# Kernel tuning notes

Measured on AMD Instinct MI355X. Metric: run time of the kernel, lower is better.

## Reference

```python
import jax, jax.numpy as jnp
import numpy as np

EPS = 1e-6


def layernorm(x, w, b):
    m = jnp.mean(x, axis=-1, keepdims=True)
    v = jnp.var(x, axis=-1, keepdims=True)
    return (x - m) * jax.lax.rsqrt(v + EPS) * w + b


def rotate_half(x):
    x1, x2 = jnp.split(x, 2, axis=-1)
    return jnp.concatenate((-x2, x1), axis=-1)


def setup_inputs() -> dict:
    key = jax.random.key(0)
    ks = jax.random.split(key, 16)
    T, D, H, HD, I = 16384, 1280, 16, 80, 5120
    NSEG = 16
    inp = {
        "hidden_states": jax.random.normal(ks[0], (T, D), jnp.float32),
        "cos": jax.random.uniform(ks[1], (T, HD), jnp.float32),
        "sin": jax.random.uniform(ks[2], (T, HD), jnp.float32),
        "ln1_w": jnp.ones((D,), jnp.float32),
        "ln1_b": jnp.zeros((D,), jnp.float32),
        "ln2_w": jnp.ones((D,), jnp.float32),
        "ln2_b": jnp.zeros((D,), jnp.float32),
        "qkv_w": jax.random.normal(ks[3], (3 * D, D), jnp.float32) * 0.02,
        "qkv_b": jnp.zeros((3 * D,), jnp.float32),
        "proj_w": jax.random.normal(ks[4], (D, D), jnp.float32) * 0.02,
        "proj_b": jnp.zeros((D,), jnp.float32),
        "fc1_w": jax.random.normal(ks[5], (I, D), jnp.float32) * 0.02,
        "fc1_b": jnp.zeros((I,), jnp.float32),
        "fc2_w": jax.random.normal(ks[6], (D, I), jnp.float32) * 0.02,
        "fc2_b": jnp.zeros((D,), jnp.float32),
        "cu_seqlens": jnp.arange(NSEG + 1, dtype=jnp.int32) * (T // NSEG),
    }
    return inp


def reference(hidden_states, cos, sin, ln1_w, ln1_b, ln2_w, ln2_b,
              qkv_w, qkv_b, proj_w, proj_b, fc1_w, fc1_b, fc2_w, fc2_b,
              cu_seqlens):
    T, D = hidden_states.shape
    H = 16
    HD = D // H
    nseg = cu_seqlens.shape[0] - 1  # equal-length segments by construction
    L = T // nseg

    x = layernorm(hidden_states, ln1_w, ln1_b)
    qkv = (x @ qkv_w.T + qkv_b).reshape(T, 3, H, HD)
    q, k, v = qkv[:, 0], qkv[:, 1], qkv[:, 2]  # [T, H, HD]

    # RoPE in fp32, cos/sin broadcast over heads
    c = cos[:, None, :]
    s = sin[:, None, :]
    q = q * c + rotate_half(q) * s
    k = k * c + rotate_half(k) * s

    # block-diagonal varlen attention: reshape into [nseg, L, H, HD]
    qs = q.reshape(nseg, L, H, HD)
    ks = k.reshape(nseg, L, H, HD)
    vs = v.reshape(nseg, L, H, HD)
    scale = 1.0 / jnp.sqrt(jnp.asarray(HD, jnp.float32))
    scores = jnp.einsum('slhd,smhd->shlm', qs, ks) * scale
    probs = jax.nn.softmax(scores, axis=-1)
    attn = jnp.einsum('shlm,smhd->slhd', probs, vs).reshape(T, D)

    attn_out = attn @ proj_w.T + proj_b
    h = hidden_states + attn_out

    y = layernorm(h, ln2_w, ln2_b)
    mlp = (jax.nn.silu(y @ fc1_w.T + fc1_b)) @ fc2_w.T + fc2_b
    return h + mlp
```

## Files before the change

kernel.cpp:

```cpp
#include <hip/hip_runtime.h>
#include <hip/hip_bf16.h>
#include <hip/hip_fp16.h>

typedef _Float16 f16;
typedef _Float16 f16x2 __attribute__((ext_vector_type(2)));
typedef _Float16 f16x4 __attribute__((ext_vector_type(4)));
typedef _Float16 f16x8 __attribute__((ext_vector_type(8)));
typedef float f32x4 __attribute__((ext_vector_type(4)));
typedef float f32x16 __attribute__((ext_vector_type(16)));
typedef int i32x4 __attribute__((ext_vector_type(4)));

#define T_TOK 16384
#define D_MOD 1280
#define N_QKV 3840
#define I_MLP 5120
#define N_HEAD 16
#define HD 80
#define SEG_L 1024

__device__ __forceinline__ void async16(const void* g, void* l) {
    __builtin_amdgcn_global_load_lds(
        (const __attribute__((address_space(1))) void*)g,
        (__attribute__((address_space(3))) void*)l, 16, 0, 0);
}

#define BAR()        asm volatile("s_barrier" ::: "memory")
#define WAIT_LGKM0() do { asm volatile("s_waitcnt lgkmcnt(0)" ::: "memory"); \
                          __builtin_amdgcn_sched_barrier(0); } while (0)
#define WAIT_VM(n)   asm volatile("s_waitcnt vmcnt(" #n ")" ::: "memory")
#define SCHED0()     __builtin_amdgcn_sched_barrier(0)

__device__ __forceinline__ int f2i(f16x2 v) { int r; __builtin_memcpy(&r, &v, 4); return r; }

__global__ __launch_bounds__(256) void cast_f32_f16(
    const float* __restrict__ src, f16* __restrict__ dst, int n) {
    int i = blockIdx.x * 256 + threadIdx.x;
    if (i < n) dst[i] = (f16)src[i];
}

template <typename TIN>
__global__ __launch_bounds__(256) void ln_kernel(
    const TIN* __restrict__ x, const float* __restrict__ w,
    const float* __restrict__ b, f16* __restrict__ out) {
    const int t = blockIdx.x;
    const TIN* row = x + (size_t)t * D_MOD;
    float vals[5];
    float s = 0.f, s2 = 0.f;
    for (int i = 0; i < 5; ++i) {
        float v = (float)row[threadIdx.x + i * 256];
        vals[i] = v; s += v; s2 += v * v;
    }
    for (int off = 32; off > 0; off >>= 1) {
        s  += __shfl_down(s, off);
        s2 += __shfl_down(s2, off);
    }
    __shared__ float rs[4], rs2[4];
    int wv = threadIdx.x >> 6;
    if ((threadIdx.x & 63) == 0) { rs[wv] = s; rs2[wv] = s2; }
    __syncthreads();
    s  = rs[0] + rs[1] + rs[2] + rs[3];
    s2 = rs2[0] + rs2[1] + rs2[2] + rs2[3];
    float m = s * (1.f / D_MOD);
    float var = s2 * (1.f / D_MOD) - m * m;
    float rstd = rsqrtf(var + 1e-6f);
    for (int i = 0; i < 5; ++i) {
        int c = threadIdx.x + i * 256;
        out[(size_t)t * D_MOD + c] = (f16)((vals[i] - m) * rstd * w[c] + b[c]);
    }
}

__global__ __launch_bounds__(256) void rope_inplace(
    f16* __restrict__ q, f16* __restrict__ k,
    const float* __restrict__ cosb, const float* __restrict__ sinb) {
    int i = blockIdx.x * 256 + threadIdx.x;
    if (i >= T_TOK * N_HEAD * 40) return;
    int d = i % 40;
    int th = i / 40;
    int h = th & 15;
    int t = th >> 4;
    size_t i0 = ((size_t)h * T_TOK + t) * HD + d;
    size_t i1 = i0 + 40;
    float c0 = cosb[t * HD + d],      s0 = sinb[t * HD + d];
    float c1 = cosb[t * HD + d + 40], s1 = sinb[t * HD + d + 40];
    {
        float x0 = (float)q[i0], x1 = (float)q[i1];
        q[i0] = (f16)(x0 * c0 - x1 * s0);
        q[i1] = (f16)(x1 * c1 + x0 * s1);
    }
    {
        float x0 = (float)k[i0], x1 = (float)k[i1];
        k[i0] = (f16)(x0 * c0 - x1 * s0);
        k[i1] = (f16)(x1 * c1 + x0 * s1);
    }
}

#define EPI_QKV   0
#define EPI_PROJ  1
#define EPI_SILU  2
#define EPI_FC2A  3
#define EPI_FC2B  4

#define RD_A(DST, MH, BUF) \
    _Pragma("unroll") for (int mi = 0; mi < 4; ++mi) { \
        const f16* pa = &LB[BUF][MH][(wr * 64 + mi * 16 + lane16) * 64]; \
        DST[mi][0] = *(const f16x8*)&pa[ch0]; \
        DST[mi][1] = *(const f16x8*)&pa[ch1]; \
    }
#define RD_B(DST, NH, BUF) \
    _Pragma("unroll") for (int ni = 0; ni < 2; ++ni) { \
        const f16* pb = &LB[BUF][2 + NH][(wc * 32 + ni * 16 + lane16) * 64]; \
        DST[ni][0] = *(const f16x8*)&pb[ch0]; \
        DST[ni][1] = *(const f16x8*)&pb[ch1]; \
    }
#define MFMA_PH(MH, NH, AARR, BARR) \
    __builtin_amdgcn_s_setprio(1); \
    _Pragma("unroll") for (int h2 = 0; h2 < 2; ++h2) \
    _Pragma("unroll") for (int mi = 0; mi < 4; ++mi) \
    _Pragma("unroll") for (int ni = 0; ni < 2; ++ni) \
        acc[MH][NH][mi][ni] = __builtin_amdgcn_mfma_f32_16x16x32_f16( \
            AARR[mi][h2], BARR[ni][h2], acc[MH][NH][mi][ni], 0, 0, 0); \
    __builtin_amdgcn_s_setprio(0);

template <int EPI>
__global__ __launch_bounds__(512, 2) void gemm_bt(
    const f16* __restrict__ A, const f16* __restrict__ B,
    const float* __restrict__ bias, const void* __restrict__ resid,
    void* __restrict__ out0, f16* __restrict__ out1, f16* __restrict__ out2,
    int M, int N, int K, int lda, int ldb, int ldo) {
    __shared__ __align__(16) f16 LB[2][4][8192];
    const int tid = threadIdx.x;
    const int w = tid >> 6;
    const int l = tid & 63;
    const int lane16 = l & 15, quad = l >> 4;
    const int wr = w >> 2, wc = w & 3;

    const int nx = gridDim.x;
    int id = blockIdx.y * nx + blockIdx.x;
    const int nwg = nx * gridDim.y;
    int tile = ((nwg & 7) == 0) ? ((id & 7) * (nwg >> 3) + (id >> 3)) : id;
    const int m0 = (tile / nx) * 256;
    const int n0 = (tile % nx) * 256;
    const int NT = K >> 6;

    const int rr = tid >> 3;
    const int cc = (tid & 7) ^ (rr & 7);
    const size_t ga_off = (size_t)rr * lda + cc * 8;
    const size_t gb_off = (size_t)rr * ldb + cc * 8;
    const int lds_off = w * 512;
    const int swz = lane16 & 7;
    const int ch0 = ((0 * 4 + quad) ^ swz) * 8;
    const int ch1 = ((1 * 4 + quad) ^ swz) * 8;

    f32x4 acc[2][2][4][2];
#pragma unroll
    for (int a = 0; a < 2; ++a)
#pragma unroll
        for (int b2 = 0; b2 < 2; ++b2)
#pragma unroll
            for (int c = 0; c < 4; ++c)
#pragma unroll
                for (int d = 0; d < 2; ++d)
                    acc[a][b2][c][d] = (f32x4){0.f, 0.f, 0.f, 0.f};

    const f16* Abase = A + (size_t)m0 * lda;
    const f16* Bbase = B + (size_t)n0 * ldb;
    auto stageA = [&](int buf, int ph, int t) {
        const f16* g = Abase + (size_t)(ph * 128) * lda + (size_t)t * 64 + ga_off;
        f16* lr = &LB[buf][ph][0] + lds_off;
        async16(g, lr);
        async16(g + (size_t)64 * lda, lr + 4096);
    };
    auto stageB = [&](int buf, int ph, int t) {
        const f16* g = Bbase + (size_t)(ph * 128) * ldb + (size_t)t * 64 + gb_off;
        f16* lr = &LB[buf][2 + ph][0] + lds_off;
        async16(g, lr);
        async16(g + (size_t)64 * ldb, lr + 4096);
    };

    f16x8 aF0[4][2], aF1[4][2], bF0[2][2], bF1[2][2];

    stageA(0, 0, 0); stageB(0, 0, 0); stageB(0, 1, 0); stageA(0, 1, 0);
    if (NT > 1) { stageA(1, 0, 1); stageB(1, 0, 1); stageB(1, 1, 1); stageA(1, 1, 1); }
    WAIT_VM(0);
    BAR();
    RD_A(aF0, 0, 0);
    WAIT_LGKM0();
    BAR();

    for (int t = 0; t < NT; ++t) {
        const int lb = t & 1;
        RD_B(bF0, 0, lb);
        RD_B(bF1, 1, lb);
        if (t + 2 < NT) stageA(lb, 0, t + 2);
        SCHED0();
        MFMA_PH(0, 0, aF0, bF0);
        WAIT_LGKM0(); BAR();
        RD_A(aF1, 1, lb);
        if (t + 2 < NT) stageB(lb, 1, t + 2);
        SCHED0();
        MFMA_PH(0, 1, aF0, bF1);
        WAIT_LGKM0(); BAR();
        if (t + 2 < NT) stageA(lb, 1, t + 2);
        if (t < NT - 2) { WAIT_VM(6); } else { WAIT_VM(0); }
        SCHED0();
        MFMA_PH(1, 1, aF1, bF1);
        WAIT_LGKM0(); BAR();
        if (t + 2 < NT) stageB(lb, 0, t + 2);
        if (t + 1 < NT) RD_A(aF0, 0, lb ^ 1);
        SCHED0();
        MFMA_PH(1, 0, aF1, bF0);
        WAIT_LGKM0(); BAR();
    }

#pragma unroll
    for (int mh = 0; mh < 2; ++mh)
#pragma unroll
    for (int mi = 0; mi < 4; ++mi) {
        const int row = m0 + mh * 128 + wr * 64 + mi * 16 + quad * 4;
#pragma unroll
        for (int nh = 0; nh < 2; ++nh)
#pragma unroll
        for (int ni = 0; ni < 2; ++ni) {
            const int col = n0 + nh * 128 + wc * 32 + ni * 16 + lane16;
            const f32x4 v4 = acc[mh][nh][mi][ni];
            float bv = (EPI == EPI_FC2B) ? 0.f : bias[col];
            if (EPI == EPI_QKV) {
                int g = col / D_MOD;
                int rem = col - g * D_MOD;
                int h = rem / HD, d = rem - h * HD;
                if (g == 2) {
                    f16x4 pk;
#pragma unroll
                    for (int r2 = 0; r2 < 4; ++r2) pk[r2] = (f16)(v4[r2] + bv);
                    f16* dst = out2 + ((size_t)h * HD + d) * T_TOK + row;
                    *(f16x4*)dst = pk;
                } else {
                    f16* dst = (g == 0) ? (f16*)out0 : out1;
                    size_t base = ((size_t)h * T_TOK) * HD + d;
#pragma unroll
                    for (int r2 = 0; r2 < 4; ++r2) {
                        float v = v4[r2] + bv;
                        dst[base + (size_t)(row + r2) * HD] = (f16)v;
                    }
                }
            } else {
#pragma unroll
                for (int r2 = 0; r2 < 4; ++r2) {
                    float v = v4[r2] + bv;
                    size_t idx = (size_t)(row + r2) * ldo + col;
                    if (EPI == EPI_PROJ) {
                        ((f16*)out0)[idx] = (f16)(v + ((const float*)resid)[idx]);
                    } else if (EPI == EPI_SILU) {
                        ((f16*)out0)[idx] = (f16)(v / (1.f + __expf(-v)));
                    } else if (EPI == EPI_FC2A) {
                        ((float*)out0)[idx] = v + (float)((const f16*)resid)[idx];
                    } else {
                        ((float*)out0)[idx] += v;
                    }
                }
            }
        }
    }
}

#undef RD_A
#undef RD_B
#undef MFMA_PH

__global__ __launch_bounds__(256, 2) void attn_kernel(
    const f16* __restrict__ q, const f16* __restrict__ k,
    const f16* __restrict__ vt, f16* __restrict__ out) {
    const int bid0 = blockIdx.x;
    const int bid = (bid0 & 7) * 256 + (bid0 >> 3);
    const int s = bid >> 7, h = (bid >> 3) & 15, qt = bid & 7;
    const int t0 = s * SEG_L;
    const int tid = threadIdx.x;
    const int w = tid >> 6, l = tid & 63;
    const int l31 = l & 31, hi = l >> 5;

    __shared__ __align__(16) f16 lK[64 * 128];
    __shared__ __align__(16) f16 lVt[96 * 64];
    __shared__ float lInv[128];

    const f16 scale = (f16)0.16132167f;

    const int qrow_g = t0 + qt * 128 + w * 32 + l31;
    const f16* qp = q + ((size_t)h * T_TOK + qrow_g) * HD;
    f16x8 qf[5];
#pragma unroll
    for (int ks = 0; ks < 5; ++ks) {
        f16x8 v = *(const f16x8*)&qp[(ks * 2 + hi) * 8];
        qf[ks] = v * scale;
    }

    const f16* kbase  = k  + (size_t)h * T_TOK * HD + (size_t)t0 * HD;
    const f16* vtbase = vt + (size_t)h * HD * T_TOK + t0;

    if (tid < 128) {
        int r = 80 + (tid >> 3), c = tid & 7;
        *(f16x8*)&lVt[r * 64 + ((c ^ (r & 7)) * 8)] = (f16x8){0,0,0,0,0,0,0,0};
    }

    f16x8 kreg[3], vreg[3];
    auto ld_tile = [&](int kt) {
#pragma unroll
        for (int j = 0; j < 3; ++j) {
            int idx = tid + j * 256;
            if (idx < 640) {
                int r = idx / 10, c = idx - r * 10;
                kreg[j] = *(const f16x8*)&kbase[(size_t)(kt * 64 + r) * HD + c * 8];
                int rv = idx >> 3, cv = idx & 7;
                vreg[j] = *(const f16x8*)&vtbase[(size_t)rv * T_TOK + kt * 64 + cv * 8];
            }
        }
    };
    auto st_tile = [&]() {
#pragma unroll
        for (int j = 0; j < 3; ++j) {
            int idx = tid + j * 256;
            if (idx < 640) {
                int r = idx / 10, c = idx - r * 10;
                *(f16x8*)&lK[r * 128 + ((c ^ (r & 7)) * 8)] = kreg[j];
                int rv = idx >> 3, cv = idx & 7;
                *(f16x8*)&lVt[rv * 64 + ((cv ^ (rv & 7)) * 8)] = vreg[j];
            }
        }
    };

    float lrow = 0.f;
    f32x16 zz;
#pragma unroll
    for (int i = 0; i < 16; ++i) zz[i] = 0.f;
    f32x16 oacc[3];
    oacc[0] = zz; oacc[1] = zz; oacc[2] = zz;

    ld_tile(0);
    st_tile();
    __syncthreads();

    for (int kt = 0; kt < 16; ++kt) {
        if (kt < 15) ld_tile(kt + 1);

#pragma unroll
        for (int ct = 0; ct < 2; ++ct) {
            f32x16 sc = zz;
#pragma unroll
            for (int ks = 0; ks < 5; ++ks) {
                const int row = ct * 32 + l31;
                f16x8 kf = *(const f16x8*)&lK[row * 128 +
                              (((ks * 2 + hi) ^ (l31 & 7)) * 8)];
                sc = __builtin_amdgcn_mfma_f32_32x32x16_f16(kf, qf[ks], sc, 0, 0, 0);
            }
            float pf[16];
#pragma unroll
            for (int r = 0; r < 16; ++r) {
                float p = __builtin_exp2f(fminf(sc[r], 14.f));
                lrow += p;
                pf[r] = p;
            }
            f16x2 own[4][2];
            int prt[4][2];
#pragma unroll
            for (int d = 0; d < 4; ++d) {
                own[d][0] = (f16x2){(f16)pf[4 * d + 0], (f16)pf[4 * d + 1]};
                own[d][1] = (f16x2){(f16)pf[4 * d + 2], (f16)pf[4 * d + 3]};
                prt[d][0] = __shfl_xor(f2i(own[d][0]), 32);
                prt[d][1] = __shfl_xor(f2i(own[d][1]), 32);
            }
#pragma unroll
            for (int kk2 = 0; kk2 < 2; ++kk2) {
                const int De = 2 * kk2, Do = 2 * kk2 + 1;
                i32x4 av;
                av[0] = hi ? prt[Do][0] : f2i(own[De][0]);
                av[1] = hi ? prt[Do][1] : f2i(own[De][1]);
                av[2] = hi ? f2i(own[Do][0]) : prt[De][0];
                av[3] = hi ? f2i(own[Do][1]) : prt[De][1];
                f16x8 af;
                __builtin_memcpy(&af, &av, 16);
                const int kkg = ct * 2 + kk2;
#pragma unroll
                for (int nt = 0; nt < 3; ++nt) {
                    const int vrow = nt * 32 + l31;
                    f16x8 vf = *(const f16x8*)&lVt[vrow * 64 +
                                  (((kkg * 2 + hi) ^ (l31 & 7)) * 8)];
                    oacc[nt] = __builtin_amdgcn_mfma_f32_32x32x16_f16(
                        af, vf, oacc[nt], 0, 0, 0);
                }
            }
        }
        __syncthreads();
        if (kt < 15) st_tile();
        __syncthreads();
    }

    lrow += __shfl_xor(lrow, 32);
    float inv = 1.f / lrow;
    lInv[w * 32 + l31] = inv;

    f16* obase = out + (size_t)(t0 + qt * 128 + w * 32) * D_MOD + h * HD;
#pragma unroll
    for (int nt = 0; nt < 3; ++nt) {
        const int hd = nt * 32 + l31;
        if (nt < 2 || l31 < 16) {
#pragma unroll
            for (int r = 0; r < 16; ++r) {
                const int qrow = (r & 3) + 8 * (r >> 2) + 4 * hi;
                obase[(size_t)qrow * D_MOD + hd] =
                    (f16)(oacc[nt][r] * lInv[w * 32 + qrow]);
            }
        }
    }
}

extern "C" void kernel_launch(void* const* d_in, const int* in_sizes, int n_in,
                              void* d_out, int out_size, void* d_ws, size_t ws_size,
                              hipStream_t stream) {
    const float* hidden = (const float*)d_in[0];
    const float* cosb   = (const float*)d_in[1];
    const float* sinb   = (const float*)d_in[2];
    const float* ln1w   = (const float*)d_in[3];
    const float* ln1b   = (const float*)d_in[4];
    const float* ln2w   = (const float*)d_in[5];
    const float* ln2b   = (const float*)d_in[6];
    const float* qkvw   = (const float*)d_in[7];
    const float* qkvb   = (const float*)d_in[8];
    const float* projw  = (const float*)d_in[9];
    const float* projb  = (const float*)d_in[10];
    const float* fc1w   = (const float*)d_in[11];
    const float* fc1b   = (const float*)d_in[12];
    const float* fc2w   = (const float*)d_in[13];
    const float* fc2b   = (const float*)d_in[14];
    float* out = (float*)d_out;

    f16* wqkv  = (f16*)d_ws;
    f16* wproj = wqkv  + 4915200;
    f16* wfc1  = wproj + 1638400;
    f16* wfc2  = wfc1  + 6553600;
    f16* qf    = wfc2  + 6553600;
    f16* kf    = qf    + 20971520;
    f16* vf    = kf    + 20971520;
    f16* xf    = vf    + 20971520;
    f16* hbuf  = xf    + 20971520;
    f16* attnf  = xf;
    f16* yf     = qf;
    f16* fc1out = kf;

    cast_f32_f16<<<(4915200 + 255) / 256, 256, 0, stream>>>(qkvw, wqkv, 4915200);
    cast_f32_f16<<<(1638400 + 255) / 256, 256, 0, stream>>>(projw, wproj, 1638400);
    cast_f32_f16<<<(6553600 + 255) / 256, 256, 0, stream>>>(fc1w, wfc1, 6553600);
    cast_f32_f16<<<(6553600 + 255) / 256, 256, 0, stream>>>(fc2w, wfc2, 6553600);

    ln_kernel<float><<<T_TOK, 256, 0, stream>>>(hidden, ln1w, ln1b, xf);

    gemm_bt<EPI_QKV><<<dim3(N_QKV / 256, T_TOK / 256), 512, 0, stream>>>(
        xf, wqkv, qkvb, nullptr, qf, kf, vf,
        T_TOK, N_QKV, D_MOD, D_MOD, D_MOD, 0);

    rope_inplace<<<(T_TOK * N_HEAD * 40) / 256, 256, 0, stream>>>(qf, kf, cosb, sinb);

    attn_kernel<<<2048, 256, 0, stream>>>(qf, kf, vf, attnf);

    gemm_bt<EPI_PROJ><<<dim3(D_MOD / 256, T_TOK / 256), 512, 0, stream>>>(
        attnf, wproj, projb, hidden, hbuf, nullptr, nullptr,
        T_TOK, D_MOD, D_MOD, D_MOD, D_MOD, D_MOD);

    ln_kernel<f16><<<T_TOK, 256, 0, stream>>>(hbuf, ln2w, ln2b, yf);

    for (int c = 0; c < 2; ++c) {
        gemm_bt<EPI_SILU><<<dim3(2560 / 256, T_TOK / 256), 512, 0, stream>>>(
            yf, wfc1 + (size_t)c * 2560 * D_MOD, fc1b + c * 2560, nullptr,
            fc1out, nullptr, nullptr,
            T_TOK, 2560, D_MOD, D_MOD, D_MOD, 2560);
        if (c == 0) {
            gemm_bt<EPI_FC2A><<<dim3(D_MOD / 256, T_TOK / 256), 512, 0, stream>>>(
                fc1out, wfc2, fc2b, hbuf, out, nullptr, nullptr,
                T_TOK, D_MOD, 2560, 2560, I_MLP, D_MOD);
        } else {
            gemm_bt<EPI_FC2B><<<dim3(D_MOD / 256, T_TOK / 256), 512, 0, stream>>>(
                fc1out, wfc2 + 2560, fc2b, nullptr, out, nullptr, nullptr,
                T_TOK, D_MOD, 2560, 2560, I_MLP, D_MOD);
        }
    }
}
```

Before: 1.405 ms.

## Split-K proj and FC2 GEMMs with atomic accumulation into fp32 residual buffer

The proj and FC2 GEMMs, which have only 5 N-tiles, now use a split-K grid dimension (z=2) with atomicAdd epilogues. This doubles the number of workgroups and improves CU occupancy. The residual and bias are pre-added into an fp32 buffer by a new vectorised add_bias kernel, and LN2 now reads that fp32 h. It also replaces the sched_barrier calls in the GEMM main loop with full s_barriers and reorders the A-fragment read. Costs are atomic traffic to global memory, extra passes over the fp32 buffers, and nondeterministic summation order.

```diff
diff --git a/kernel.cpp b/kernel.cpp
--- a/kernel.cpp
+++ b/kernel.cpp
@@ -28,7 +28,6 @@
 #define WAIT_LGKM0() do { asm volatile("s_waitcnt lgkmcnt(0)" ::: "memory"); \
                           __builtin_amdgcn_sched_barrier(0); } while (0)
 #define WAIT_VM(n)   asm volatile("s_waitcnt vmcnt(" #n ")" ::: "memory")
-#define SCHED0()     __builtin_amdgcn_sched_barrier(0)
 
 __device__ __forceinline__ int f2i(f16x2 v) { int r; __builtin_memcpy(&r, &v, 4); return r; }
 
@@ -36,6 +35,18 @@
     const float* __restrict__ src, f16* __restrict__ dst, int n) {
     int i = blockIdx.x * 256 + threadIdx.x;
     if (i < n) dst[i] = (f16)src[i];
+}
+
+__global__ __launch_bounds__(256) void add_bias_f32(
+    const float* __restrict__ src, const float* __restrict__ bias,
+    float* __restrict__ dst) {
+    const int n4 = T_TOK * D_MOD / 4;
+    for (int i = blockIdx.x * 256 + threadIdx.x; i < n4; i += gridDim.x * 256) {
+        f32x4 s = ((const f32x4*)src)[i];
+        int col = (i * 4) % D_MOD;
+        f32x4 b = *(const f32x4*)&bias[col];
+        ((f32x4*)dst)[i] = s + b;
+    }
 }
 
 template <typename TIN>
@@ -95,10 +106,8 @@
 }
 
 #define EPI_QKV   0
-#define EPI_PROJ  1
 #define EPI_SILU  2
-#define EPI_FC2A  3
-#define EPI_FC2B  4
+#define EPI_ACC   5
 
 #define RD_A(DST, MH, BUF) \
     _Pragma("unroll") for (int mi = 0; mi < 4; ++mi) { \
@@ -124,7 +133,7 @@
 template <int EPI>
 __global__ __launch_bounds__(512, 2) void gemm_bt(
     const f16* __restrict__ A, const f16* __restrict__ B,
-    const float* __restrict__ bias, const void* __restrict__ resid,
+    const float* __restrict__ bias,
     void* __restrict__ out0, f16* __restrict__ out1, f16* __restrict__ out2,
     int M, int N, int K, int lda, int ldb, int ldo) {
     __shared__ __align__(16) f16 LB[2][4][8192];
@@ -134,12 +143,16 @@
     const int lane16 = l & 15, quad = l >> 4;
     const int wr = w >> 2, wc = w & 3;
 
-    const int nx = gridDim.x;
-    int id = blockIdx.y * nx + blockIdx.x;
-    const int nwg = nx * gridDim.y;
+    const int nx = gridDim.x, ny = gridDim.y;
+    const int nxy = nx * ny;
+    int id = (blockIdx.z * ny + blockIdx.y) * nx + blockIdx.x;
+    const int nwg = nxy * gridDim.z;
     int tile = ((nwg & 7) == 0) ? ((id & 7) * (nwg >> 3) + (id >> 3)) : id;
-    const int m0 = (tile / nx) * 256;
-    const int n0 = (tile % nx) * 256;
+    const int zi = tile / nxy;
+    const int rem = tile - zi * nxy;
+    const int m0 = (rem / nx) * 256;
+    const int n0 = (rem % nx) * 256;
+    const int kbase = zi * K;
     const int NT = K >> 6;
 
     const int rr = tid >> 3;
@@ -162,8 +175,8 @@
                 for (int d = 0; d < 2; ++d)
                     acc[a][b2][c][d] = (f32x4){0.f, 0.f, 0.f, 0.f};
 
-    const f16* Abase = A + (size_t)m0 * lda;
-    const f16* Bbase = B + (size_t)n0 * ldb;
+    const f16* Abase = A + (size_t)m0 * lda + kbase;
+    const f16* Bbase = B + (size_t)n0 * ldb + kbase;
     auto stageA = [&](int buf, int ph, int t) {
         const f16* g = Abase + (size_t)(ph * 128) * lda + (size_t)t * 64 + ga_off;
         f16* lr = &LB[buf][ph][0] + lds_off;
@@ -192,22 +205,22 @@
         RD_B(bF0, 0, lb);
         RD_B(bF1, 1, lb);
         if (t + 2 < NT) stageA(lb, 0, t + 2);
-        SCHED0();
+        BAR();
         MFMA_PH(0, 0, aF0, bF0);
         WAIT_LGKM0(); BAR();
         RD_A(aF1, 1, lb);
         if (t + 2 < NT) stageB(lb, 1, t + 2);
-        SCHED0();
+        BAR();
         MFMA_PH(0, 1, aF0, bF1);
         WAIT_LGKM0(); BAR();
         if (t + 2 < NT) stageA(lb, 1, t + 2);
         if (t < NT - 2) { WAIT_VM(6); } else { WAIT_VM(0); }
-        SCHED0();
+        BAR();
         MFMA_PH(1, 1, aF1, bF1);
         WAIT_LGKM0(); BAR();
+        if (t + 1 < NT) RD_A(aF0, 0, lb ^ 1);
         if (t + 2 < NT) stageB(lb, 0, t + 2);
-        if (t + 1 < NT) RD_A(aF0, 0, lb ^ 1);
-        SCHED0();
+        BAR();
         MFMA_PH(1, 0, aF1, bF0);
         WAIT_LGKM0(); BAR();
     }
@@ -223,11 +236,11 @@
         for (int ni = 0; ni < 2; ++ni) {
             const int col = n0 + nh * 128 + wc * 32 + ni * 16 + lane16;
             const f32x4 v4 = acc[mh][nh][mi][ni];
-            float bv = (EPI == EPI_FC2B) ? 0.f : bias[col];
+            float bv = (EPI == EPI_ACC) ? 0.f : bias[col];
             if (EPI == EPI_QKV) {
                 int g = col / D_MOD;
-                int rem = col - g * D_MOD;
-                int h = rem / HD, d = rem - h * HD;
+                int rem2 = col - g * D_MOD;
+                int h = rem2 / HD, d = rem2 - h * HD;
                 if (g == 2) {
                     f16x4 pk;
 #pragma unroll
@@ -243,20 +256,18 @@
                         dst[base + (size_t)(row + r2) * HD] = (f16)v;
                     }
                 }
-            } else {
+            } else if (EPI == EPI_SILU) {
 #pragma unroll
                 for (int r2 = 0; r2 < 4; ++r2) {
                     float v = v4[r2] + bv;
                     size_t idx = (size_t)(row + r2) * ldo + col;
-                    if (EPI == EPI_PROJ) {
-                        ((f16*)out0)[idx] = (f16)(v + ((const float*)resid)[idx]);
-                    } else if (EPI == EPI_SILU) {
-                        ((f16*)out0)[idx] = (f16)(v / (1.f + __expf(-v)));
-                    } else if (EPI == EPI_FC2A) {
-                        ((float*)out0)[idx] = v + (float)((const f16*)resid)[idx];
-                    } else {
-                        ((float*)out0)[idx] += v;
-                    }
+                    ((f16*)out0)[idx] = (f16)(v / (1.f + __expf(-v)));
+                }
+            } else {
+#pragma unroll
+                for (int r2 = 0; r2 < 4; ++r2) {
+                    size_t idx = (size_t)(row + r2) * ldo + col;
+                    atomicAdd((float*)out0 + idx, v4[r2]);
                 }
             }
         }
@@ -443,7 +454,8 @@
     f16* hbuf  = xf    + 20971520;
     f16* attnf  = xf;
     f16* yf     = qf;
-    f16* fc1out = kf;
+    float* h32  = (float*)kf;
+    f16* fc1out = xf;
 
     cast_f32_f16<<<(4915200 + 255) / 256, 256, 0, stream>>>(qkvw, wqkv, 4915200);
     cast_f32_f16<<<(1638400 + 255) / 256, 256, 0, stream>>>(projw, wproj, 1638400);
@@ -452,33 +464,30 @@
 
     ln_kernel<float><<<T_TOK, 256, 0, stream>>>(hidden, ln1w, ln1b, xf);
 
-    gemm_bt<EPI_QKV><<<dim3(N_QKV / 256, T_TOK / 256), 512, 0, stream>>>(
-        xf, wqkv, qkvb, nullptr, qf, kf, vf,
+    gemm_bt<EPI_QKV><<<dim3(N_QKV / 256, T_TOK / 256, 1), 512, 0, stream>>>(
+        xf, wqkv, qkvb, qf, kf, vf,
         T_TOK, N_QKV, D_MOD, D_MOD, D_MOD, 0);
 
     rope_inplace<<<(T_TOK * N_HEAD * 40) / 256, 256, 0, stream>>>(qf, kf, cosb, sinb);
 
     attn_kernel<<<2048, 256, 0, stream>>>(qf, kf, vf, attnf);
 
-    gemm_bt<EPI_PROJ><<<dim3(D_MOD / 256, T_TOK / 256), 512, 0, stream>>>(
-        attnf, wproj, projb, hidden, hbuf, nullptr, nullptr,
-        T_TOK, D_MOD, D_MOD, D_MOD, D_MOD, D_MOD);
-
-    ln_kernel<f16><<<T_TOK, 256, 0, stream>>>(hbuf, ln2w, ln2b, yf);
+    add_bias_f32<<<2048, 256, 0, stream>>>(hidden, projb, h32);
+    gemm_bt<EPI_ACC><<<dim3(D_MOD / 256, T_TOK / 256, 2), 512, 0, stream>>>(
+        attnf, wproj, nullptr, h32, nullptr, nullptr,
+        T_TOK, D_MOD, D_MOD / 2, D_MOD, D_MOD, D_MOD);
+
+    ln_kernel<float><<<T_TOK, 256, 0, stream>>>(h32, ln2w, ln2b, yf);
+
+    add_bias_f32<<<2048, 256, 0, stream>>>(h32, fc2b, out);
 
     for (int c = 0; c < 2; ++c) {
-        gemm_bt<EPI_SILU><<<dim3(2560 / 256, T_TOK / 256), 512, 0, stream>>>(
-            yf, wfc1 + (size_t)c * 2560 * D_MOD, fc1b + c * 2560, nullptr,
+        gemm_bt<EPI_SILU><<<dim3(2560 / 256, T_TOK / 256, 1), 512, 0, stream>>>(
+            yf, wfc1 + (size_t)c * 2560 * D_MOD, fc1b + c * 2560,
             fc1out, nullptr, nullptr,
             T_TOK, 2560, D_MOD, D_MOD, D_MOD, 2560);
-        if (c == 0) {
-            gemm_bt<EPI_FC2A><<<dim3(D_MOD / 256, T_TOK / 256), 512, 0, stream>>>(
-                fc1out, wfc2, fc2b, hbuf, out, nullptr, nullptr,
-                T_TOK, D_MOD, 2560, 2560, I_MLP, D_MOD);
-        } else {
-            gemm_bt<EPI_FC2B><<<dim3(D_MOD / 256, T_TOK / 256), 512, 0, stream>>>(
-                fc1out, wfc2 + 2560, fc2b, nullptr, out, nullptr, nullptr,
-                T_TOK, D_MOD, 2560, 2560, I_MLP, D_MOD);
-        }
-    }
-}
+        gemm_bt<EPI_ACC><<<dim3(D_MOD / 256, T_TOK / 256, 2), 512, 0, stream>>>(
+            fc1out, wfc2 + (size_t)c * 2560, nullptr, out, nullptr, nullptr,
+            T_TOK, D_MOD, 2560 / 2, 2560, I_MLP, D_MOD);
+    }
+}
```

New measurement: 1.636 ms. +16.5%, slower.
